# Performance work log

Hardware: AMD Instinct MI355X
Metric: run time of the kernel (lower is better)

The kernel has to match this reference:

```python
import jax, jax.numpy as jnp
import numpy as np

DT_RANK = 160
D_STATE = 16


def setup_inputs() -> dict:
    key = jax.random.key(0)
    ks = jax.random.split(key, 13)
    B, D, E = 32, 2560, 5120
    s = lambda k, shape, sc=0.02: (jax.random.normal(k, shape, dtype=jnp.float32) * sc)
    return {
        "x": jax.random.normal(ks[0], (1, 1, B, D), dtype=jnp.float32),
        "W_in_ssm": s(ks[1], (D, E)),
        "W_in_mlp": s(ks[2], (D, E)),
        "W_out": s(ks[3], (E, D)),
        "conv_w": s(ks[4], (4, B, E), 0.1),
        "conv_b": s(ks[5], (B, E), 0.1),
        "conv_states": jax.random.normal(ks[6], (3, 1, 1, B, E), dtype=jnp.float32),
        "Wx": s(ks[7], (E, DT_RANK + 2 * D_STATE)),
        "W_dt": s(ks[8], (DT_RANK, E)),
        "dt_bias": s(ks[9], (E,), 0.5),
        "A_log": jax.random.uniform(ks[10], (E, D_STATE), dtype=jnp.float32),
        "D": s(ks[11], (E,), 1.0),
        "h": jax.random.normal(ks[12], (B, E, D_STATE), dtype=jnp.float32) * 0.1,
    }


def reference(x, W_in_ssm, W_in_mlp, W_out, conv_w, conv_b, conv_states, Wx, W_dt, dt_bias, A_log, D, h):
    # x: [1,1,B,d_model]
    x_ssm = x @ W_in_ssm  # [1,1,B,E]
    # FIFO: 3 carried conv states + newest projection -> 4 taps
    states = jnp.concatenate([conv_states, x_ssm[None]], axis=0)  # [4,1,1,B,E]
    # unrolled 4-tap causal depthwise conv (per-batch-broadcast weights) + bias + SiLU
    conv = jnp.einsum('tabne,tne->abne', states, conv_w) + conv_b  # [1,1,B,E]
    conv = jax.nn.silu(conv)

    # --- single-step selective SSM (Mamba decode) ---
    xt = conv[0, 0]  # [B,E]
    dbc = xt @ Wx  # [B, dt_rank + 2*d_state]
    dt = jax.nn.softplus(dbc[:, :DT_RANK] @ W_dt + dt_bias)  # [B,E]
    Bm = dbc[:, DT_RANK:DT_RANK + D_STATE]  # [B,N]
    Cm = dbc[:, DT_RANK + D_STATE:]         # [B,N]
    A = -jnp.exp(A_log)                      # [E,N]
    dA = jnp.exp(dt[:, :, None] * A[None])   # [B,E,N]
    h_new = h * dA + (dt[:, :, None] * Bm[:, None, :]) * xt[:, :, None]
    y = jnp.einsum('ben,bn->be', h_new, Cm) + D * xt  # [B,E]
    y = y[None, None]  # [1,1,B,E]

    # gated residual branch: silu-activated mlp projection
    residual = jax.nn.silu(x @ W_in_mlp)  # [1,1,B,E]
    out = y * residual
    return out @ W_out  # [1,1,B,d_model]
```

## Files before the change

### kernel.cpp

```cpp
#include <hip/hip_runtime.h>
#include <math.h>

#define EE 5120
#define DD 2560
#define BB 32

__device__ __forceinline__ void g2l16(const float* g, float* l) {
  __builtin_amdgcn_global_load_lds(
      (const __attribute__((address_space(1))) void*)g,
      (__attribute__((address_space(3))) void*)l, 16, 0, 0);
}

__global__ __launch_bounds__(256) void k0_prep(const float* __restrict__ x,
                                               float* __restrict__ xT,
                                               float* __restrict__ dbc) {
  int g = blockIdx.x * 256 + threadIdx.x;
  if (g < BB * DD) {
    int b = g / DD, k = g % DD;
    xT[k * BB + b] = x[g];
  }
  if (g < BB * 192) dbc[g] = 0.f;
}

__global__ __launch_bounds__(256) void gemm_sk(const float* __restrict__ W0,
                                               const float* __restrict__ W1,
                                               int wsplit, int wstride,
                                               const float* __restrict__ xsrc,
                                               float* __restrict__ P,
                                               int pstride, int ncb) {
  __shared__ float smem[10240];
  const int cb   = blockIdx.x % ncb;
  const int so   = blockIdx.x / ncb;
  const int lane = threadIdx.x & 63;
  const int wv   = __builtin_amdgcn_readfirstlane((int)(threadIdx.x >> 6));
  const int c0   = cb * 64;
  const float* __restrict__ W = (c0 < wsplit) ? W0 : W1;
  const int wc0  = (c0 < wsplit) ? c0 : c0 - wsplit;
  const int kw   = so * 320 + wv * 80;

  float acc[BB];
#pragma unroll
  for (int b = 0; b < BB; ++b) acc[b] = 0.f;

  float* stage = smem + wv * 2560;
  const int rg = lane >> 4;
  const int cg = (lane & 15) * 4;

  for (int ch = 0; ch < 2; ++ch) {
    const int kc = kw + ch * 40;
    __builtin_amdgcn_s_waitcnt(0);
#pragma unroll
    for (int j = 0; j < 10; ++j) {
      const float* g = W + (size_t)(kc + j * 4 + rg) * wstride + wc0 + cg;
      g2l16(g, stage + (j * 4) * 64);
    }
    __builtin_amdgcn_s_waitcnt(0);
    const float* __restrict__ xrow = xsrc + (size_t)kc * BB;
#pragma unroll 4
    for (int kk = 0; kk < 40; ++kk) {
      float w = stage[kk * 64 + lane];
#pragma unroll
      for (int b = 0; b < BB; ++b)
        acc[b] = fmaf(xrow[kk * BB + b], w, acc[b]);
    }
  }

#pragma unroll
  for (int half = 0; half < 2; ++half) {
    __syncthreads();
#pragma unroll
    for (int i = 0; i < 16; ++i)
      smem[(wv * 64 + lane) * 17 + i] = acc[half * 16 + i];
    __syncthreads();
#pragma unroll
    for (int j = 0; j < 4; ++j) {
      int bi = wv * 4 + j;
      float v = smem[(0 * 64 + lane) * 17 + bi] + smem[(1 * 64 + lane) * 17 + bi] +
                smem[(2 * 64 + lane) * 17 + bi] + smem[(3 * 64 + lane) * 17 + bi];
      int b = half * 16 + bi;
      P[((size_t)(so * BB + b)) * pstride + c0 + lane] = v;
    }
  }
}

__global__ __launch_bounds__(256) void k1b_epilogue(const float* __restrict__ P1,
                                                    const float* __restrict__ cs,
                                                    const float* __restrict__ cw,
                                                    const float* __restrict__ cbv,
                                                    float* __restrict__ xt,
                                                    float* __restrict__ res) {
  int g = blockIdx.x * 256 + threadIdx.x;
  int e = g % EE;
  int b = g / EE;
  float xs = 0.f, xm = 0.f;
#pragma unroll
  for (int so = 0; so < 8; ++so) {
    xs += P1[((size_t)(so * BB + b)) * 10240 + e];
    xm += P1[((size_t)(so * BB + b)) * 10240 + EE + e];
  }
  size_t be = (size_t)b * EE + e;
  const size_t T = (size_t)BB * EE;
  float conv = cs[be] * cw[be] + cs[T + be] * cw[T + be] +
               cs[2 * T + be] * cw[2 * T + be] + xs * cw[3 * T + be] + cbv[be];
  float sig = 1.f / (1.f + expf(-conv));
  xt[be] = conv * sig;
  float sm = 1.f / (1.f + expf(-xm));
  res[be] = xm * sm;
}

__global__ __launch_bounds__(256) void k2_dbc(const float* __restrict__ xt,
                                              const float* __restrict__ Wx,
                                              float* __restrict__ dbc) {
  const int bid  = blockIdx.x;
  const int cbi  = bid % 3;
  const int so   = bid / 3;
  const int lane = threadIdx.x & 63;
  const int j    = cbi * 64 + lane;
  const int k0   = so * 80 + (int)(threadIdx.x >> 6) * 20;

  float acc[BB];
#pragma unroll
  for (int b = 0; b < BB; ++b) acc[b] = 0.f;

  for (int kk = 0; kk < 20; kk += 4) {
    int k = k0 + kk;
    float w0 = Wx[(size_t)(k + 0) * 192 + j];
    float w1 = Wx[(size_t)(k + 1) * 192 + j];
    float w2 = Wx[(size_t)(k + 2) * 192 + j];
    float w3 = Wx[(size_t)(k + 3) * 192 + j];
#pragma unroll
    for (int b = 0; b < BB; ++b) acc[b] = fmaf(xt[(size_t)b * EE + k + 0], w0, acc[b]);
#pragma unroll
    for (int b = 0; b < BB; ++b) acc[b] = fmaf(xt[(size_t)b * EE + k + 1], w1, acc[b]);
#pragma unroll
    for (int b = 0; b < BB; ++b) acc[b] = fmaf(xt[(size_t)b * EE + k + 2], w2, acc[b]);
#pragma unroll
    for (int b = 0; b < BB; ++b) acc[b] = fmaf(xt[(size_t)b * EE + k + 3], w3, acc[b]);
  }

  __shared__ float red[4][64][17];
  const int ksid = threadIdx.x >> 6;
#pragma unroll
  for (int half = 0; half < 2; ++half) {
    __syncthreads();
#pragma unroll
    for (int i = 0; i < 16; ++i) red[ksid][lane][i] = acc[half * 16 + i];
    __syncthreads();
#pragma unroll
    for (int jj = 0; jj < 4; ++jj) {
      int bi = ksid * 4 + jj;
      float v = red[0][lane][bi] + red[1][lane][bi] +
                red[2][lane][bi] + red[3][lane][bi];
      int b = half * 16 + bi;
      atomicAdd(&dbc[b * 192 + j], v);
    }
  }
}

__global__ __launch_bounds__(256) void k3_ssm(const float* __restrict__ dbc,
                                              const float* __restrict__ Wdt,
                                              const float* __restrict__ dt_bias,
                                              const float* __restrict__ A_log,
                                              const float* __restrict__ Dvec,
                                              const float* __restrict__ h,
                                              const float* __restrict__ xt,
                                              const float* __restrict__ res,
                                              float* __restrict__ zT) {
  __shared__ float sw[10240];
  const int eb   = blockIdx.x % 80;
  const int bg   = blockIdx.x / 80;
  const int lane = threadIdx.x & 63;
  const int wv   = __builtin_amdgcn_readfirstlane((int)(threadIdx.x >> 6));
  const int e    = eb * 64 + lane;
  const int bq   = bg * 4 + wv;
  const int b0   = bq * 2, b1 = b0 + 1;

  {
    const int rg = lane >> 4, cg = (lane & 15) * 4;
#pragma unroll
    for (int j = 0; j < 10; ++j) {
      int r = wv * 40 + j * 4 + rg;
      g2l16(Wdt + (size_t)r * EE + eb * 64 + cg, sw + (wv * 40 + j * 4) * 64);
    }
  }
  __syncthreads();

  float a0 = 0.f, a1 = 0.f;
  const float* __restrict__ d0 = dbc + b0 * 192;
  const float* __restrict__ d1 = dbc + b1 * 192;
#pragma unroll 4
  for (int r = 0; r < 160; ++r) {
    float w = sw[r * 64 + lane];
    a0 = fmaf(d0[r], w, a0);
    a1 = fmaf(d1[r], w, a1);
  }

  float An[16];
#pragma unroll
  for (int n = 0; n < 16; ++n) An[n] = -expf(A_log[e * 16 + n]);
  const float bias = dt_bias[e];
  const float Dv = Dvec[e];

#pragma unroll
  for (int t = 0; t < 2; ++t) {
    int b = t ? b1 : b0;
    float a = t ? a1 : a0;
    float v = a + bias;
    float dt = (v > 20.f) ? v : log1pf(expf(v));
    size_t be = (size_t)b * EE + e;
    float xb = xt[be];
    const float* __restrict__ hb = h + be * 16;
    const float* __restrict__ Bm = dbc + b * 192 + 160;
    const float* __restrict__ Cm = dbc + b * 192 + 176;
    float y = 0.f;
#pragma unroll
    for (int n = 0; n < 16; ++n) {
      float dA = expf(dt * An[n]);
      float hn = fmaf(hb[n], dA, dt * Bm[n] * xb);
      y = fmaf(hn, Cm[n], y);
    }
    y = fmaf(Dv, xb, y);
    zT[e * BB + b] = y * res[be];
  }
}

__global__ __launch_bounds__(256) void k4b_reduce(const float* __restrict__ P4,
                                                  float* __restrict__ out) {
  int g = blockIdx.x * 256 + threadIdx.x;
  int d = g % DD;
  int b = g / DD;
  float s = 0.f;
#pragma unroll
  for (int so = 0; so < 16; ++so) s += P4[((size_t)(so * BB + b)) * DD + d];
  out[g] = s;
}

extern "C" void kernel_launch(void* const* d_in, const int* in_sizes, int n_in,
                              void* d_out, int out_size, void* d_ws, size_t ws_size,
                              hipStream_t stream) {
  const float* x       = (const float*)d_in[0];
  const float* Wssm    = (const float*)d_in[1];
  const float* Wmlp    = (const float*)d_in[2];
  const float* Wout    = (const float*)d_in[3];
  const float* conv_w  = (const float*)d_in[4];
  const float* conv_b  = (const float*)d_in[5];
  const float* conv_st = (const float*)d_in[6];
  const float* Wx      = (const float*)d_in[7];
  const float* Wdt     = (const float*)d_in[8];
  const float* dt_bias = (const float*)d_in[9];
  const float* A_log   = (const float*)d_in[10];
  const float* Dvec    = (const float*)d_in[11];
  const float* h       = (const float*)d_in[12];
  float* out = (float*)d_out;

  float* ws = (float*)d_ws;
  float* xT  = ws;
  float* P1  = xT  + 81920;
  float* xt  = P1  + 2621440;
  float* res = xt  + 163840;
  float* dbc = res + 163840;
  float* zT  = dbc + 6144;
  float* P4  = zT  + 163840;

  hipLaunchKernelGGL(k0_prep,     dim3(320),  dim3(256), 0, stream, x, xT, dbc);
  hipLaunchKernelGGL(gemm_sk,     dim3(1280), dim3(256), 0, stream,
                     Wssm, Wmlp, EE, EE, xT, P1, 10240, 160);
  hipLaunchKernelGGL(k1b_epilogue,dim3(640),  dim3(256), 0, stream, P1, conv_st, conv_w, conv_b, xt, res);
  hipLaunchKernelGGL(k2_dbc,      dim3(192),  dim3(256), 0, stream, xt, Wx, dbc);
  hipLaunchKernelGGL(k3_ssm,      dim3(320),  dim3(256), 0, stream, dbc, Wdt, dt_bias, A_log, Dvec, h, xt, res, zT);
  hipLaunchKernelGGL(gemm_sk,     dim3(640),  dim3(256), 0, stream,
                     Wout, Wout, 1 << 30, DD, zT, P4, DD, 40);
  hipLaunchKernelGGL(k4b_reduce,  dim3(320),  dim3(256), 0, stream, P4, out);
}
```

Measured before the change: 271.6 us.

## Replace scalar FMA split-K GEMM with split-bf16 MFMA matrix-core GEMM

The weight-streaming GEMMs (input projections and output projection) move from per-lane scalar FMAs over LDS-staged weights to 32x32x16 bf16 MFMA instructions. Each fp32 operand is split into high and low bf16 halves and three MFMAs per step (hi*hi, lo*hi, hi*lo) approximate fp32 accuracy. Weights are now loaded directly from global memory into registers with double buffering instead of going through global_load_lds staging, and the output row mapping follows the MFMA accumulator layout. The aim is to cut ALU time so the kernel becomes purely bandwidth bound. The cost is some precision loss and strided per-lane global loads, which may coalesce less well than the previous LDS path.

```diff
diff --git a/kernel.cpp b/kernel.cpp
--- a/kernel.cpp
+++ b/kernel.cpp
@@ -4,6 +4,21 @@
 #define EE 5120
 #define DD 2560
 #define BB 32
+
+typedef __attribute__((ext_vector_type(8)))  short  short8;
+typedef __attribute__((ext_vector_type(8)))  __bf16 bf16x8;
+typedef __attribute__((ext_vector_type(16))) float  f32x16;
+
+__device__ __forceinline__ void split8(const float* v, short8& hi, short8& lo) {
+#pragma unroll
+  for (int j = 0; j < 8; ++j) {
+    unsigned u = __float_as_uint(v[j]);
+    hi[j] = (short)(u >> 16);
+    float r = v[j] - __uint_as_float(u & 0xFFFF0000u);
+    lo[j] = (short)(__float_as_uint(r) >> 16);
+  }
+}
+#define BC(x) __builtin_bit_cast(bf16x8, x)
 
 __device__ __forceinline__ void g2l16(const float* g, float* l) {
   __builtin_amdgcn_global_load_lds(
@@ -22,13 +37,13 @@
   if (g < BB * 192) dbc[g] = 0.f;
 }
 
-__global__ __launch_bounds__(256) void gemm_sk(const float* __restrict__ W0,
-                                               const float* __restrict__ W1,
-                                               int wsplit, int wstride,
-                                               const float* __restrict__ xsrc,
-                                               float* __restrict__ P,
-                                               int pstride, int ncb) {
-  __shared__ float smem[10240];
+__global__ __launch_bounds__(256) void gemm_mfma(const float* __restrict__ W0,
+                                                 const float* __restrict__ W1,
+                                                 int wsplit, int wstride,
+                                                 const float* __restrict__ xsrc,
+                                                 float* __restrict__ P,
+                                                 int pstride, int ncb) {
+  __shared__ float red[4 * 64 * 17];
   const int cb   = blockIdx.x % ncb;
   const int so   = blockIdx.x / ncb;
   const int lane = threadIdx.x & 63;
@@ -37,48 +52,58 @@
   const float* __restrict__ W = (c0 < wsplit) ? W0 : W1;
   const int wc0  = (c0 < wsplit) ? c0 : c0 - wsplit;
   const int kw   = so * 320 + wv * 80;
-
-  float acc[BB];
-#pragma unroll
-  for (int b = 0; b < BB; ++b) acc[b] = 0.f;
-
-  float* stage = smem + wv * 2560;
-  const int rg = lane >> 4;
-  const int cg = (lane & 15) * 4;
-
-  for (int ch = 0; ch < 2; ++ch) {
-    const int kc = kw + ch * 40;
-    __builtin_amdgcn_s_waitcnt(0);
-#pragma unroll
-    for (int j = 0; j < 10; ++j) {
-      const float* g = W + (size_t)(kc + j * 4 + rg) * wstride + wc0 + cg;
-      g2l16(g, stage + (j * 4) * 64);
-    }
-    __builtin_amdgcn_s_waitcnt(0);
-    const float* __restrict__ xrow = xsrc + (size_t)kc * BB;
-#pragma unroll 4
-    for (int kk = 0; kk < 40; ++kk) {
-      float w = stage[kk * 64 + lane];
-#pragma unroll
-      for (int b = 0; b < BB; ++b)
-        acc[b] = fmaf(xrow[kk * BB + b], w, acc[b]);
-    }
-  }
-
-#pragma unroll
-  for (int half = 0; half < 2; ++half) {
-    __syncthreads();
-#pragma unroll
-    for (int i = 0; i < 16; ++i)
-      smem[(wv * 64 + lane) * 17 + i] = acc[half * 16 + i];
-    __syncthreads();
-#pragma unroll
-    for (int j = 0; j < 4; ++j) {
-      int bi = wv * 4 + j;
-      float v = smem[(0 * 64 + lane) * 17 + bi] + smem[(1 * 64 + lane) * 17 + bi] +
-                smem[(2 * 64 + lane) * 17 + bi] + smem[(3 * 64 + lane) * 17 + bi];
-      int b = half * 16 + bi;
-      P[((size_t)(so * BB + b)) * pstride + c0 + lane] = v;
+  const int kl   = (lane >> 5) * 8;
+  const int ln   = lane & 31;
+
+  float av[5][8];
+#pragma unroll
+  for (int s = 0; s < 5; ++s)
+#pragma unroll
+    for (int j = 0; j < 8; ++j)
+      av[s][j] = xsrc[(size_t)(kw + s * 16 + kl + j) * BB + ln];
+  short8 ah[5], al[5];
+#pragma unroll
+  for (int s = 0; s < 5; ++s) split8(av[s], ah[s], al[s]);
+
+#pragma unroll
+  for (int t = 0; t < 2; ++t) {
+    f32x16 acc;
+#pragma unroll
+    for (int i = 0; i < 16; ++i) acc[i] = 0.f;
+
+    const float* __restrict__ wp =
+        W + (size_t)kw * wstride + wc0 + t * 32 + ln;
+
+    float bv0[8], bv1[8];
+#pragma unroll
+    for (int j = 0; j < 8; ++j) bv0[j] = wp[(size_t)(kl + j) * wstride];
+#pragma unroll
+    for (int s = 0; s < 5; ++s) {
+      float (&cur)[8] = (s & 1) ? bv1 : bv0;
+      float (&nxt)[8] = (s & 1) ? bv0 : bv1;
+      if (s < 4) {
+#pragma unroll
+        for (int j = 0; j < 8; ++j)
+          nxt[j] = wp[(size_t)((s + 1) * 16 + kl + j) * wstride];
+      }
+      short8 bh, bl;
+      split8(cur, bh, bl);
+      acc = __builtin_amdgcn_mfma_f32_32x32x16_bf16(BC(ah[s]), BC(bh), acc, 0, 0, 0);
+      acc = __builtin_amdgcn_mfma_f32_32x32x16_bf16(BC(al[s]), BC(bh), acc, 0, 0, 0);
+      acc = __builtin_amdgcn_mfma_f32_32x32x16_bf16(BC(ah[s]), BC(bl), acc, 0, 0, 0);
+    }
+
+    __syncthreads();
+#pragma unroll
+    for (int r = 0; r < 16; ++r) red[(wv * 64 + lane) * 17 + r] = acc[r];
+    __syncthreads();
+#pragma unroll
+    for (int q = 0; q < 4; ++q) {
+      int r = wv * 4 + q;
+      float sum = red[(0 * 64 + lane) * 17 + r] + red[(1 * 64 + lane) * 17 + r] +
+                  red[(2 * 64 + lane) * 17 + r] + red[(3 * 64 + lane) * 17 + r];
+      int row = (r & 3) + 8 * (r >> 2) + 4 * (lane >> 5);
+      P[((size_t)(so * 32 + row)) * pstride + c0 + t * 32 + ln] = sum;
     }
   }
 }
@@ -138,19 +163,19 @@
     for (int b = 0; b < BB; ++b) acc[b] = fmaf(xt[(size_t)b * EE + k + 3], w3, acc[b]);
   }
 
-  __shared__ float red[4][64][17];
+  __shared__ float red2[4][64][17];
   const int ksid = threadIdx.x >> 6;
 #pragma unroll
   for (int half = 0; half < 2; ++half) {
     __syncthreads();
 #pragma unroll
-    for (int i = 0; i < 16; ++i) red[ksid][lane][i] = acc[half * 16 + i];
+    for (int i = 0; i < 16; ++i) red2[ksid][lane][i] = acc[half * 16 + i];
     __syncthreads();
 #pragma unroll
     for (int jj = 0; jj < 4; ++jj) {
       int bi = ksid * 4 + jj;
-      float v = red[0][lane][bi] + red[1][lane][bi] +
-                red[2][lane][bi] + red[3][lane][bi];
+      float v = red2[0][lane][bi] + red2[1][lane][bi] +
+                red2[2][lane][bi] + red2[3][lane][bi];
       int b = half * 16 + bi;
       atomicAdd(&dbc[b * 192 + j], v);
     }
@@ -263,12 +288,12 @@
   float* P4  = zT  + 163840;
 
   hipLaunchKernelGGL(k0_prep,     dim3(320),  dim3(256), 0, stream, x, xT, dbc);
-  hipLaunchKernelGGL(gemm_sk,     dim3(1280), dim3(256), 0, stream,
+  hipLaunchKernelGGL(gemm_mfma,   dim3(1280), dim3(256), 0, stream,
                      Wssm, Wmlp, EE, EE, xT, P1, 10240, 160);
   hipLaunchKernelGGL(k1b_epilogue,dim3(640),  dim3(256), 0, stream, P1, conv_st, conv_w, conv_b, xt, res);
   hipLaunchKernelGGL(k2_dbc,      dim3(192),  dim3(256), 0, stream, xt, Wx, dbc);
   hipLaunchKernelGGL(k3_ssm,      dim3(320),  dim3(256), 0, stream, dbc, Wdt, dt_bias, A_log, Dvec, h, xt, res, zT);
-  hipLaunchKernelGGL(gemm_sk,     dim3(640),  dim3(256), 0, stream,
+  hipLaunchKernelGGL(gemm_mfma,   dim3(640),  dim3(256), 0, stream,
                      Wout, Wout, 1 << 30, DD, zT, P4, DD, 40);
   hipLaunchKernelGGL(k4b_reduce,  dim3(320),  dim3(256), 0, stream, P4, out);
 }
```

Measured after the change: 249.5 us. 8.2% less time.
